# Performance work log

Hardware: AMD Instinct MI355X
Metric: run time of the kernel (lower is better)

The kernel has to match this reference:

```python
import jax, jax.numpy as jnp
import numpy as np

H_HEADS = 8

def _conv1x1(x, w):
    # x: (b, C_in, H, W), w: (C_out, C_in, 1, 1)
    return jax.lax.conv_general_dilated(
        x, w, window_strides=(1, 1), padding='VALID',
        dimension_numbers=('NCHW', 'OIHW', 'NCHW'))

def setup_inputs() -> dict:
    key = jax.random.key(0)
    kx, kq, kk, kv = jax.random.split(key, 4)
    x = jax.random.normal(kx, (16, 256, 64, 64), dtype=jnp.float32)
    sc = 1.0 / np.sqrt(256.0)
    wq = jax.random.normal(kq, (256, 256, 1, 1), dtype=jnp.float32) * sc
    wk = jax.random.normal(kk, (256, 256, 1, 1), dtype=jnp.float32) * sc
    wv = jax.random.normal(kv, (256, 256, 1, 1), dtype=jnp.float32) * sc
    return {"x": x, "wq": wq, "wk": wk, "wv": wv}

def reference(x, wq, wk, wv):
    b, _, Hs, Ws = x.shape
    h = H_HEADS
    v = _conv1x1(x, wv)                      # (b, C, H, W)
    C = v.shape[1]
    d = C // h
    q = _conv1x1(x, wq).reshape(b, h, d, -1)  # (b, h, d, N)
    k = _conv1x1(x, wk).reshape(b, h, d, -1)
    vflat = v.reshape(b, h, d, -1)
    # channel-attention: contract over spatial N -> (b, h, d, d)
    scores = jnp.einsum('bhdn,bhen->bhde', q, k) / jnp.sqrt(jnp.float32(h))
    attn_weights = jax.nn.softmax(scores, axis=-1)
    attn = jnp.einsum('bhde,bhen->bhdn', attn_weights, vflat)  # (b, h, d, N)
    # ChannelShuffle(groups=h): (b, h, d, H, W) -> (b, d, h, H, W) -> (b, C, H, W)
    shuffled = attn.reshape(b, h, d, Hs, Ws).transpose(0, 2, 1, 3, 4).reshape(b, C, Hs, Ws)
    out = shuffled + v
    return (out, attn_weights)
```

## Files before the change

### kernel.cpp

```cpp
#include <hip/hip_runtime.h>
#include <hip/hip_bf16.h>
#include <stdint.h>

typedef __attribute__((ext_vector_type(4))) float f32x4;
typedef __attribute__((ext_vector_type(8))) short bf16x8;
typedef __attribute__((ext_vector_type(4))) short bf16x4;
typedef __attribute__((ext_vector_type(4))) unsigned int u32x4;

__device__ __forceinline__ unsigned short f2bf_rne(float f) {
  union { float f; unsigned int u; } v; v.f = f;
  unsigned int r = v.u + 0x7FFFu + ((v.u >> 16) & 1u);
  return (unsigned short)(r >> 16);
}
__device__ __forceinline__ float bf2f(unsigned short s) {
  union { float f; unsigned int u; } v; v.u = ((unsigned int)s) << 16;
  return v.f;
}

__global__ __launch_bounds__(512, 4) void k_gram(const float* __restrict__ x,
                                                 float* __restrict__ Gpart) {
  __shared__ __align__(16) unsigned char lds[2][32768];
  const int b = blockIdx.y;
  const int n0 = blockIdx.x << 8;
  const int half = blockIdx.z;
  const int t = threadIdx.x;
  const int lane = t & 63;
  const int w = t >> 6;
  const int ti = (half << 1) + (w >> 2);
  const int tj = w & 3;
  const int wm = ti << 6;
  const int wn = tj << 6;
  const int row_ld = t >> 1;
  const int nh = t & 1;
  const int lrow = lane & 15;
  const int lkg = lane >> 4;

  f32x4 acc[4][4];
#pragma unroll
  for (int i = 0; i < 4; i++)
#pragma unroll
    for (int j = 0; j < 4; j++) acc[i][j] = (f32x4){0.f, 0.f, 0.f, 0.f};

  const float* gx = x + (((size_t)(b * 256 + row_ld)) << 12) + n0 + (nh << 4);

  for (int sub = 0; sub < 8; sub++) {
    unsigned char* buf = lds[sub & 1];
    f32x4 v0 = *(const f32x4*)(gx + (sub << 5));
    f32x4 v1 = *(const f32x4*)(gx + (sub << 5) + 4);
    f32x4 v2 = *(const f32x4*)(gx + (sub << 5) + 8);
    f32x4 v3 = *(const f32x4*)(gx + (sub << 5) + 12);
    float vv[16] = {v0[0], v0[1], v0[2], v0[3], v1[0], v1[1], v1[2], v1[3],
                    v2[0], v2[1], v2[2], v2[3], v3[0], v3[1], v3[2], v3[3]};
    unsigned short hi[16], lo[16];
#pragma unroll
    for (int j = 0; j < 16; j++) {
      hi[j] = f2bf_rne(vv[j]);
      lo[j] = f2bf_rne(vv[j] - bf2f(hi[j]));
    }
    u32x4 hw0 = {(unsigned)hi[0] | ((unsigned)hi[1] << 16),
                 (unsigned)hi[2] | ((unsigned)hi[3] << 16),
                 (unsigned)hi[4] | ((unsigned)hi[5] << 16),
                 (unsigned)hi[6] | ((unsigned)hi[7] << 16)};
    u32x4 hw1 = {(unsigned)hi[8] | ((unsigned)hi[9] << 16),
                 (unsigned)hi[10] | ((unsigned)hi[11] << 16),
                 (unsigned)hi[12] | ((unsigned)hi[13] << 16),
                 (unsigned)hi[14] | ((unsigned)hi[15] << 16)};
    u32x4 lw0 = {(unsigned)lo[0] | ((unsigned)lo[1] << 16),
                 (unsigned)lo[2] | ((unsigned)lo[3] << 16),
                 (unsigned)lo[4] | ((unsigned)lo[5] << 16),
                 (unsigned)lo[6] | ((unsigned)lo[7] << 16)};
    u32x4 lw1 = {(unsigned)lo[8] | ((unsigned)lo[9] << 16),
                 (unsigned)lo[10] | ((unsigned)lo[11] << 16),
                 (unsigned)lo[12] | ((unsigned)lo[13] << 16),
                 (unsigned)lo[14] | ((unsigned)lo[15] << 16)};
    const int swz = (row_ld & 7) << 4;
    unsigned char* rbase = buf + row_ld * 128;
    *(u32x4*)(rbase + (((nh << 5)) ^ swz)) = hw0;
    *(u32x4*)(rbase + (((nh << 5) + 16) ^ swz)) = hw1;
    *(u32x4*)(rbase + ((64 + (nh << 5)) ^ swz)) = lw0;
    *(u32x4*)(rbase + ((64 + (nh << 5) + 16) ^ swz)) = lw1;
    __syncthreads();

    bf16x8 bh[4], bl[4];
#pragma unroll
    for (int nf = 0; nf < 4; nf++) {
      int col = wn + (nf << 4) + lrow;
      int cs = (col & 7) << 4;
      bh[nf] = *(const bf16x8*)(buf + col * 128 + (((lkg << 4)) ^ cs));
      bl[nf] = *(const bf16x8*)(buf + col * 128 + ((64 + (lkg << 4)) ^ cs));
    }
#pragma unroll
    for (int mf = 0; mf < 4; mf++) {
      int row = wm + (mf << 4) + lrow;
      int rs = (row & 7) << 4;
      bf16x8 ah = *(const bf16x8*)(buf + row * 128 + (((lkg << 4)) ^ rs));
      bf16x8 al = *(const bf16x8*)(buf + row * 128 + ((64 + (lkg << 4)) ^ rs));
#pragma unroll
      for (int nf = 0; nf < 4; nf++) {
        acc[mf][nf] = __builtin_amdgcn_mfma_f32_16x16x32_bf16(ah, bh[nf], acc[mf][nf], 0, 0, 0);
        acc[mf][nf] = __builtin_amdgcn_mfma_f32_16x16x32_bf16(ah, bl[nf], acc[mf][nf], 0, 0, 0);
        acc[mf][nf] = __builtin_amdgcn_mfma_f32_16x16x32_bf16(al, bh[nf], acc[mf][nf], 0, 0, 0);
      }
    }
  }

  if (tj >= ti) {
    float* Gp = Gpart + (((size_t)(blockIdx.x * 16 + b)) << 16);
#pragma unroll
    for (int mf = 0; mf < 4; mf++)
#pragma unroll
      for (int nf = 0; nf < 4; nf++) {
        int col = wn + (nf << 4) + lrow;
#pragma unroll
        for (int r = 0; r < 4; r++) {
          int row = wm + (mf << 4) + (lkg << 2) + r;
          Gp[row * 256 + col] = acc[mf][nf][r];
        }
      }
  }
}

__global__ __launch_bounds__(256) void k_reduce(const float* __restrict__ Gpart,
                                                float* __restrict__ G) {
  __shared__ float tl[16][68];
  const int bx = blockIdx.x;
  const int b = bx / 40;
  const int rem = bx % 40;
  const int tp = rem >> 2, q = rem & 3;
  const int TI[10] = {0, 0, 0, 0, 1, 1, 1, 2, 2, 3};
  const int TJ[10] = {0, 1, 2, 3, 1, 2, 3, 2, 3, 3};
  const int i = TI[tp], j = TJ[tp];
  const int t = threadIdx.x;
  const int r = t >> 4, cq = t & 15;
  const int row = i * 64 + (q << 4) + r;

  const float* src = Gpart + ((size_t)b << 16) + (size_t)row * 256 + j * 64 + (cq << 2);
  f32x4 s = *(const f32x4*)(src);
#pragma unroll
  for (int ch = 1; ch < 16; ch++)
    s += *(const f32x4*)(src + (((size_t)ch) << 20));
  *(f32x4*)(G + ((size_t)b << 16) + (size_t)row * 256 + j * 64 + (cq << 2)) = s;

  if (i != j) {
    *(f32x4*)&tl[r][cq << 2] = s;
    __syncthreads();
    const int c = t >> 2, g = t & 3;
    f32x4 m;
#pragma unroll
    for (int k = 0; k < 4; k++) m[k] = tl[(g << 2) + k][c];
    *(f32x4*)(G + ((size_t)b << 16) + (size_t)(j * 64 + c) * 256 + i * 64 + (q << 4) + (g << 2)) = m;
  }
}

__global__ __launch_bounds__(512) void k_scores(const float* __restrict__ wq,
                                                const float* __restrict__ wk,
                                                const float* __restrict__ wv,
                                                const float* __restrict__ G,
                                                float* __restrict__ attn,
                                                unsigned short* __restrict__ Wout) {
  __shared__ float part[8][16][256];
  const int h = blockIdx.x, b = blockIdx.y, dg = blockIdx.z;
  const int t = threadIdx.x, lane = t & 63;
  const int wu = __builtin_amdgcn_readfirstlane(t >> 6);

  const float* wqrow = wq + (size_t)(h * 32 + dg * 16) * 256 + wu * 32;
  f32x4 tp[16];
#pragma unroll
  for (int d = 0; d < 16; d++) tp[d] = (f32x4){0.f, 0.f, 0.f, 0.f};

  const float* Gb = G + ((size_t)b << 16) + (size_t)(wu * 32) * 256 + (lane << 2);
  for (int s = 0; s < 32; s++) {
    f32x4 g = *(const f32x4*)(Gb + s * 256);
#pragma unroll
    for (int d = 0; d < 16; d++)
      tp[d] += g * wqrow[d * 256 + s];
  }
#pragma unroll
  for (int d = 0; d < 16; d++)
    *(f32x4*)&part[wu][d][lane << 2] = tp[d];
  __syncthreads();

#pragma unroll
  for (int u = 0; u < 2; u++) {
    int o = t * 2 + u;
    int d = o >> 6, q = (o & 63) << 2;
    f32x4 s = *(f32x4*)&part[0][d][q];
#pragma unroll
    for (int w2 = 1; w2 < 8; w2++) s += *(f32x4*)&part[w2][d][q];
    *(f32x4*)&part[0][d][q] = s;
  }
  __syncthreads();
  const float* Tb = &part[0][0][0];

  const int dls = t >> 5, es = t & 31;
  f32x4 sa = {0.f, 0.f, 0.f, 0.f};
  const float* Tr = Tb + dls * 256;
  const float* wkr = wk + (size_t)(h * 32 + es) * 256;
  for (int c4 = 0; c4 < 64; c4++)
    sa += *(const f32x4*)(Tr + (c4 << 2)) * *(const f32x4*)(wkr + (c4 << 2));
  float s = (sa[0] + sa[1] + sa[2] + sa[3]) * 0.35355339059327379f;

  float m = s;
#pragma unroll
  for (int off = 1; off < 32; off <<= 1) m = fmaxf(m, __shfl_xor(m, off));
  float p = expf(s - m);
  float su = p;
#pragma unroll
  for (int off = 1; off < 32; off <<= 1) su += __shfl_xor(su, off);
  float a = p / su;
  attn[(((b * 8 + h) * 32) + dg * 16 + dls) * 32 + es] = a;

  f32x4 o0 = {0.f, 0.f, 0.f, 0.f}, o1 = {0.f, 0.f, 0.f, 0.f};
  const float* wvh = wv + (size_t)(h * 32) * 256 + (lane << 2);
#pragma unroll
  for (int e = 0; e < 32; e++) {
    float a0 = __shfl(a, e);
    float a1 = __shfl(a, 32 + e);
    f32x4 vv = *(const f32x4*)(wvh + e * 256);
    o0 += vv * a0;
    o1 += vv * a1;
  }
  const int d0 = dg * 16 + 2 * wu;
  const int co0 = d0 * 8 + h, co1 = (d0 + 1) * 8 + h;
  o0 += *(const f32x4*)(wv + (size_t)co0 * 256 + (lane << 2));
  o1 += *(const f32x4*)(wv + (size_t)co1 * 256 + (lane << 2));
  bf16x4 p0, p1;
#pragma unroll
  for (int j = 0; j < 4; j++) {
    p0[j] = (short)f2bf_rne(o0[j]);
    p1[j] = (short)f2bf_rne(o1[j]);
  }
  *(bf16x4*)(Wout + ((size_t)(b * 256 + co0) << 8) + (lane << 2)) = p0;
  *(bf16x4*)(Wout + ((size_t)(b * 256 + co1) << 8) + (lane << 2)) = p1;
}

__global__ __launch_bounds__(512) void k_out(const float* __restrict__ x,
                                             const unsigned short* __restrict__ Wout,
                                             float* __restrict__ out) {
  __shared__ __align__(16) unsigned short Bt[2][4096];
  const int b = blockIdx.y;
  const int nb = blockIdx.x << 7;
  const int t = threadIdx.x;
  const int lane = t & 63;
  const int w = t >> 6;
  const int wm = (w >> 1) << 6;
  const int wn = (w & 1) << 6;
  const int lrow = lane & 15;
  const int lkg = lane >> 4;

  f32x4 acc[4][4];
#pragma unroll
  for (int i = 0; i < 4; i++)
#pragma unroll
    for (int j = 0; j < 4; j++) acc[i][j] = (f32x4){0.f, 0.f, 0.f, 0.f};

  const int pos = lane >> 3;
  const int cblk = 2 * (pos & 3) + (pos >> 2);
  const int ctil = cblk * 4 + ((lane & 7) >> 1);
  const int noff = (lane & 1) << 3;
  const float* gxb = x + (((size_t)b) << 20) + (size_t)ctil * 4096 + nb + (w << 4) + noff;
  const unsigned int bt0 = (unsigned int)(uintptr_t)(&Bt[0][0]);

  f32x4 xa = *(const f32x4*)(gxb);
  f32x4 xb = *(const f32x4*)(gxb + 4);

  for (int kt = 0; kt < 8; kt++) {
    const int p = kt & 1;
    bf16x8 pk;
#pragma unroll
    for (int j = 0; j < 4; j++) {
      pk[j] = (short)f2bf_rne(xa[j]);
      pk[4 + j] = (short)f2bf_rne(xb[j]);
    }
    *(bf16x8*)(&Bt[p][(w << 9) + (lane << 3)]) = pk;
    __syncthreads();

    if (kt < 7) {
      const float* nx = gxb + (((size_t)(kt + 1)) << 17);
      xa = *(const f32x4*)(nx);
      xb = *(const f32x4*)(nx + 4);
    }

    bf16x8 afr[4];
    const unsigned short* wrow = Wout + (((size_t)(b * 256)) << 8) + kt * 32 + (lkg << 3);
#pragma unroll
    for (int mf = 0; mf < 4; mf++) {
      int co = wm + (mf << 4) + lrow;
      afr[mf] = *(const bf16x8*)(wrow + ((size_t)co << 8));
    }

    bf16x4 t0[4], t1[4];
#pragma unroll
    for (int nf = 0; nf < 4; nf++) {
      unsigned int base = bt0 + (unsigned int)(p << 13) +
                          (unsigned int)((((wn >> 4) + nf)) << 10) + (lane << 3);
      asm volatile("ds_read_b64_tr_b16 %0, %1" : "=v"(t0[nf]) : "v"(base) : "memory");
      asm volatile("ds_read_b64_tr_b16 %0, %1 offset:512" : "=v"(t1[nf]) : "v"(base) : "memory");
    }
    asm volatile("s_waitcnt lgkmcnt(0)" ::: "memory");
    __builtin_amdgcn_sched_barrier(0);

    bf16x8 bfr[4];
#pragma unroll
    for (int nf = 0; nf < 4; nf++) {
      bfr[nf][0] = t0[nf][0]; bfr[nf][1] = t0[nf][1];
      bfr[nf][2] = t0[nf][2]; bfr[nf][3] = t0[nf][3];
      bfr[nf][4] = t1[nf][0]; bfr[nf][5] = t1[nf][1];
      bfr[nf][6] = t1[nf][2]; bfr[nf][7] = t1[nf][3];
    }
#pragma unroll
    for (int mf = 0; mf < 4; mf++)
#pragma unroll
      for (int nf = 0; nf < 4; nf++)
        acc[mf][nf] = __builtin_amdgcn_mfma_f32_16x16x32_bf16(afr[mf], bfr[nf], acc[mf][nf], 0, 0, 0);
  }

  float* ob = out + (((size_t)b) << 20) + nb;
#pragma unroll
  for (int mf = 0; mf < 4; mf++)
#pragma unroll
    for (int nf = 0; nf < 4; nf++) {
      int col = wn + (nf << 4) + lrow;
#pragma unroll
      for (int r = 0; r < 4; r++) {
        int row = wm + (mf << 4) + (lkg << 2) + r;
        ob[((size_t)row << 12) + col] = acc[mf][nf][r];
      }
    }
}

extern "C" void kernel_launch(void* const* d_in, const int* in_sizes, int n_in,
                              void* d_out, int out_size, void* d_ws, size_t ws_size,
                              hipStream_t stream) {
  const float* x = (const float*)d_in[0];
  const float* wq = (const float*)d_in[1];
  const float* wk = (const float*)d_in[2];
  const float* wv = (const float*)d_in[3];
  float* out = (float*)d_out;
  float* attn = out + (size_t)16 * 256 * 4096;

  float* Gpart = out;

  char* ws = (char*)d_ws;
  float* G = (float*)ws;
  unsigned short* Wout = (unsigned short*)(ws + (4 << 20));

  k_gram<<<dim3(16, 16, 2), dim3(512), 0, stream>>>(x, Gpart);
  k_reduce<<<dim3(640), dim3(256), 0, stream>>>(Gpart, G);
  k_scores<<<dim3(8, 16, 2), dim3(512), 0, stream>>>(wq, wk, wv, G, attn, Wout);
  k_out<<<dim3(32, 16), dim3(512), 0, stream>>>(x, Wout, out);
}
```

Measured before the change: 102.0 us.

## Halve gram partials and fuse reduce into scores via cooperative grid sync

The gram kernel now processes 512 spatial columns per block instead of 256, halving the number of partial Gram matrices (8 instead of 16) and the reduction traffic. The separate reduce and scores kernels are merged into one cooperative kernel: the first 160 blocks reduce partials into G, then a grid-wide sync precedes the scores phase. This removes one kernel launch and shrinks partial-sum memory traffic, at the cost of fewer gram blocks (less parallelism) and a grid barrier that idles most blocks during the reduction.

```diff
diff --git a/kernel.cpp b/kernel.cpp
--- a/kernel.cpp
+++ b/kernel.cpp
@@ -1,6 +1,9 @@
 #include <hip/hip_runtime.h>
 #include <hip/hip_bf16.h>
+#include <hip/hip_cooperative_groups.h>
 #include <stdint.h>
+
+namespace cg = cooperative_groups;
 
 typedef __attribute__((ext_vector_type(4))) float f32x4;
 typedef __attribute__((ext_vector_type(8))) short bf16x8;
@@ -21,7 +24,7 @@
                                                  float* __restrict__ Gpart) {
   __shared__ __align__(16) unsigned char lds[2][32768];
   const int b = blockIdx.y;
-  const int n0 = blockIdx.x << 8;
+  const int n0 = blockIdx.x << 9;
   const int half = blockIdx.z;
   const int t = threadIdx.x;
   const int lane = t & 63;
@@ -43,7 +46,7 @@
 
   const float* gx = x + (((size_t)(b * 256 + row_ld)) << 12) + n0 + (nh << 4);
 
-  for (int sub = 0; sub < 8; sub++) {
+  for (int sub = 0; sub < 16; sub++) {
     unsigned char* buf = lds[sub & 1];
     f32x4 v0 = *(const f32x4*)(gx + (sub << 5));
     f32x4 v1 = *(const f32x4*)(gx + (sub << 5) + 4);
@@ -120,47 +123,53 @@
   }
 }
 
-__global__ __launch_bounds__(256) void k_reduce(const float* __restrict__ Gpart,
-                                                float* __restrict__ G) {
-  __shared__ float tl[16][68];
+__global__ __launch_bounds__(512) void k_redscores(const float* __restrict__ wq,
+                                                   const float* __restrict__ wk,
+                                                   const float* __restrict__ wv,
+                                                   const float* __restrict__ Gpart,
+                                                   float* __restrict__ G,
+                                                   float* __restrict__ attn,
+                                                   unsigned short* __restrict__ Wout) {
+  __shared__ float part[8][16][256];
   const int bx = blockIdx.x;
-  const int b = bx / 40;
-  const int rem = bx % 40;
-  const int tp = rem >> 2, q = rem & 3;
-  const int TI[10] = {0, 0, 0, 0, 1, 1, 1, 2, 2, 3};
-  const int TJ[10] = {0, 1, 2, 3, 1, 2, 3, 2, 3, 3};
-  const int i = TI[tp], j = TJ[tp];
-  const int t = threadIdx.x;
-  const int r = t >> 4, cq = t & 15;
-  const int row = i * 64 + (q << 4) + r;
-
-  const float* src = Gpart + ((size_t)b << 16) + (size_t)row * 256 + j * 64 + (cq << 2);
-  f32x4 s = *(const f32x4*)(src);
-#pragma unroll
-  for (int ch = 1; ch < 16; ch++)
-    s += *(const f32x4*)(src + (((size_t)ch) << 20));
-  *(f32x4*)(G + ((size_t)b << 16) + (size_t)row * 256 + j * 64 + (cq << 2)) = s;
-
-  if (i != j) {
-    *(f32x4*)&tl[r][cq << 2] = s;
-    __syncthreads();
-    const int c = t >> 2, g = t & 3;
-    f32x4 m;
-#pragma unroll
-    for (int k = 0; k < 4; k++) m[k] = tl[(g << 2) + k][c];
-    *(f32x4*)(G + ((size_t)b << 16) + (size_t)(j * 64 + c) * 256 + i * 64 + (q << 4) + (g << 2)) = m;
-  }
-}
-
-__global__ __launch_bounds__(512) void k_scores(const float* __restrict__ wq,
-                                                const float* __restrict__ wk,
-                                                const float* __restrict__ wv,
-                                                const float* __restrict__ G,
-                                                float* __restrict__ attn,
-                                                unsigned short* __restrict__ Wout) {
-  __shared__ float part[8][16][256];
-  const int h = blockIdx.x, b = blockIdx.y, dg = blockIdx.z;
   const int t = threadIdx.x, lane = t & 63;
+
+  if (bx < 160) {
+    const int b = bx / 10;
+    const int tp = bx % 10;
+    const int TI[10] = {0, 0, 0, 0, 1, 1, 1, 2, 2, 3};
+    const int TJ[10] = {0, 1, 2, 3, 1, 2, 3, 2, 3, 3};
+    const int i = TI[tp], j = TJ[tp];
+    float (*tl)[68] = (float(*)[68]) & part[0][0][0];
+#pragma unroll
+    for (int u = 0; u < 2; u++) {
+      int o = t * 2 + u;
+      int r = o >> 4, cq = o & 15;
+      const float* src = Gpart + ((size_t)b << 16) + (size_t)(i * 64 + r) * 256 + j * 64 + (cq << 2);
+      f32x4 s = *(const f32x4*)src;
+#pragma unroll
+      for (int ch = 1; ch < 8; ch++)
+        s += *(const f32x4*)(src + (((size_t)ch) << 20));
+      *(f32x4*)(G + ((size_t)b << 16) + (size_t)(i * 64 + r) * 256 + j * 64 + (cq << 2)) = s;
+      if (i != j) *(f32x4*)&tl[r][cq << 2] = s;
+    }
+    if (i != j) {
+      __syncthreads();
+#pragma unroll
+      for (int u = 0; u < 2; u++) {
+        int o = t * 2 + u;
+        int c = o >> 4, g = o & 15;
+        f32x4 m;
+#pragma unroll
+        for (int q = 0; q < 4; q++) m[q] = tl[(g << 2) + q][c];
+        *(f32x4*)(G + ((size_t)b << 16) + (size_t)(j * 64 + c) * 256 + i * 64 + (g << 2)) = m;
+      }
+    }
+  }
+  __threadfence();
+  cg::this_grid().sync();
+
+  const int h = bx & 7, b = (bx >> 3) & 15, dg = bx >> 7;
   const int wu = __builtin_amdgcn_readfirstlane(t >> 6);
 
   const float* wqrow = wq + (size_t)(h * 32 + dg * 16) * 256 + wu * 32;
@@ -345,8 +354,12 @@
   float* G = (float*)ws;
   unsigned short* Wout = (unsigned short*)(ws + (4 << 20));
 
-  k_gram<<<dim3(16, 16, 2), dim3(512), 0, stream>>>(x, Gpart);
-  k_reduce<<<dim3(640), dim3(256), 0, stream>>>(Gpart, G);
-  k_scores<<<dim3(8, 16, 2), dim3(512), 0, stream>>>(wq, wk, wv, G, attn, Wout);
+  k_gram<<<dim3(8, 16, 2), dim3(512), 0, stream>>>(x, Gpart);
+
+  void* args[] = {(void*)&wq, (void*)&wk, (void*)&wv, (void*)&Gpart,
+                  (void*)&G, (void*)&attn, (void*)&Wout};
+  hipLaunchCooperativeKernel((const void*)k_redscores, dim3(256), dim3(512),
+                             args, 0, stream);
+
   k_out<<<dim3(32, 16), dim3(512), 0, stream>>>(x, Wout, out);
 }
```

Measured after the change: 211.5 us, median of 5. 2.07x slower.

## Drop reduce kernel by folding Gram partial sums into scores kernel

Applied to the files above, without the earlier changes.

Each Gram block now covers 512 spatial positions instead of 256, so there are 8 chunks per batch instead of 16. The separate reduce kernel is removed, and the scores kernel sums the 8 partial Gram matrices as it reads them. The Gram kernel now writes full 256x256 tiles, not only the upper triangle, so no transpose mirroring is needed. This saves one launch and an intermediate round trip, at the cost of half as many Gram blocks (less parallelism) and redundant partial-sum reads inside the scores kernel.

```diff
diff --git a/kernel.cpp b/kernel.cpp
--- a/kernel.cpp
+++ b/kernel.cpp
@@ -21,7 +21,7 @@
                                                  float* __restrict__ Gpart) {
   __shared__ __align__(16) unsigned char lds[2][32768];
   const int b = blockIdx.y;
-  const int n0 = blockIdx.x << 8;
+  const int n0 = blockIdx.x << 9;
   const int half = blockIdx.z;
   const int t = threadIdx.x;
   const int lane = t & 63;
@@ -43,7 +43,7 @@
 
   const float* gx = x + (((size_t)(b * 256 + row_ld)) << 12) + n0 + (nh << 4);
 
-  for (int sub = 0; sub < 8; sub++) {
+  for (int sub = 0; sub < 16; sub++) {
     unsigned char* buf = lds[sub & 1];
     f32x4 v0 = *(const f32x4*)(gx + (sub << 5));
     f32x4 v1 = *(const f32x4*)(gx + (sub << 5) + 4);
@@ -104,58 +104,24 @@
     }
   }
 
-  if (tj >= ti) {
-    float* Gp = Gpart + (((size_t)(blockIdx.x * 16 + b)) << 16);
-#pragma unroll
-    for (int mf = 0; mf < 4; mf++)
-#pragma unroll
-      for (int nf = 0; nf < 4; nf++) {
-        int col = wn + (nf << 4) + lrow;
-#pragma unroll
-        for (int r = 0; r < 4; r++) {
-          int row = wm + (mf << 4) + (lkg << 2) + r;
-          Gp[row * 256 + col] = acc[mf][nf][r];
-        }
+  float* Gp = Gpart + (((size_t)(blockIdx.x * 16 + b)) << 16);
+#pragma unroll
+  for (int mf = 0; mf < 4; mf++)
+#pragma unroll
+    for (int nf = 0; nf < 4; nf++) {
+      int col = wn + (nf << 4) + lrow;
+#pragma unroll
+      for (int r = 0; r < 4; r++) {
+        int row = wm + (mf << 4) + (lkg << 2) + r;
+        Gp[row * 256 + col] = acc[mf][nf][r];
       }
-  }
-}
-
-__global__ __launch_bounds__(256) void k_reduce(const float* __restrict__ Gpart,
-                                                float* __restrict__ G) {
-  __shared__ float tl[16][68];
-  const int bx = blockIdx.x;
-  const int b = bx / 40;
-  const int rem = bx % 40;
-  const int tp = rem >> 2, q = rem & 3;
-  const int TI[10] = {0, 0, 0, 0, 1, 1, 1, 2, 2, 3};
-  const int TJ[10] = {0, 1, 2, 3, 1, 2, 3, 2, 3, 3};
-  const int i = TI[tp], j = TJ[tp];
-  const int t = threadIdx.x;
-  const int r = t >> 4, cq = t & 15;
-  const int row = i * 64 + (q << 4) + r;
-
-  const float* src = Gpart + ((size_t)b << 16) + (size_t)row * 256 + j * 64 + (cq << 2);
-  f32x4 s = *(const f32x4*)(src);
-#pragma unroll
-  for (int ch = 1; ch < 16; ch++)
-    s += *(const f32x4*)(src + (((size_t)ch) << 20));
-  *(f32x4*)(G + ((size_t)b << 16) + (size_t)row * 256 + j * 64 + (cq << 2)) = s;
-
-  if (i != j) {
-    *(f32x4*)&tl[r][cq << 2] = s;
-    __syncthreads();
-    const int c = t >> 2, g = t & 3;
-    f32x4 m;
-#pragma unroll
-    for (int k = 0; k < 4; k++) m[k] = tl[(g << 2) + k][c];
-    *(f32x4*)(G + ((size_t)b << 16) + (size_t)(j * 64 + c) * 256 + i * 64 + (q << 4) + (g << 2)) = m;
-  }
+    }
 }
 
 __global__ __launch_bounds__(512) void k_scores(const float* __restrict__ wq,
                                                 const float* __restrict__ wk,
                                                 const float* __restrict__ wv,
-                                                const float* __restrict__ G,
+                                                const float* __restrict__ Gpart,
                                                 float* __restrict__ attn,
                                                 unsigned short* __restrict__ Wout) {
   __shared__ float part[8][16][256];
@@ -168,9 +134,12 @@
 #pragma unroll
   for (int d = 0; d < 16; d++) tp[d] = (f32x4){0.f, 0.f, 0.f, 0.f};
 
-  const float* Gb = G + ((size_t)b << 16) + (size_t)(wu * 32) * 256 + (lane << 2);
+  const float* Gb = Gpart + ((size_t)b << 16) + (size_t)(wu * 32) * 256 + (lane << 2);
   for (int s = 0; s < 32; s++) {
     f32x4 g = *(const f32x4*)(Gb + s * 256);
+#pragma unroll
+    for (int ch = 1; ch < 8; ch++)
+      g += *(const f32x4*)(Gb + (((size_t)ch) << 20) + s * 256);
 #pragma unroll
     for (int d = 0; d < 16; d++)
       tp[d] += g * wqrow[d * 256 + s];
@@ -342,11 +311,9 @@
   float* Gpart = out;
 
   char* ws = (char*)d_ws;
-  float* G = (float*)ws;
-  unsigned short* Wout = (unsigned short*)(ws + (4 << 20));
-
-  k_gram<<<dim3(16, 16, 2), dim3(512), 0, stream>>>(x, Gpart);
-  k_reduce<<<dim3(640), dim3(256), 0, stream>>>(Gpart, G);
-  k_scores<<<dim3(8, 16, 2), dim3(512), 0, stream>>>(wq, wk, wv, G, attn, Wout);
+  unsigned short* Wout = (unsigned short*)ws;
+
+  k_gram<<<dim3(8, 16, 2), dim3(512), 0, stream>>>(x, Gpart);
+  k_scores<<<dim3(8, 16, 2), dim3(512), 0, stream>>>(wq, wk, wv, Gpart, attn, Wout);
   k_out<<<dim3(32, 16), dim3(512), 0, stream>>>(x, Wout, out);
 }
```

Measured after the change: 126.5 us. +24.0%, slower.
